# Kernel tuning notes

Measured on AMD Instinct MI355X. Metric: run time of the kernel, lower is better.

Reference implementation:

```python
import jax, jax.numpy as jnp
import numpy as np

# Module constants from CheckboxDetector.__init__ / _postprocess
N = 8192            # candidate detections
C = 2               # checkbox classes (checked / unchecked)
THR = 0.7           # confidence threshold (self.threshold)
IOU_THR = 0.5       # torchvision.ops.nms iou_threshold
INPUT_H, INPUT_W = 1280.0, 1280.0   # self.input_shape
IMG_H, IMG_W = 2480.0, 3508.0       # original image (A4 @ 300dpi)
SCALER = max(IMG_W / INPUT_W, IMG_H / INPUT_H)
EPS = 1e-9


def setup_inputs() -> dict:
    key = jax.random.key(0)
    k1, k2, k3 = jax.random.split(key, 3)
    cls_conf = jax.random.uniform(k1, (N, C), dtype=jnp.float32)
    # well-formed xyxy boxes inside the 1280x1280 canvas
    xy = jax.random.uniform(k2, (N, 2), dtype=jnp.float32, minval=0.0, maxval=1200.0)
    wh = jax.random.uniform(k3, (N, 2), dtype=jnp.float32, minval=8.0, maxval=80.0)
    bboxes = jnp.concatenate([xy, xy + wh], axis=1)  # [N,4]
    return {"cls_conf": cls_conf, "bboxes": bboxes}


def _pairwise_iou(boxes):
    # boxes: [N,4] xyxy -> iou: [N,N]
    x1, y1, x2, y2 = boxes[:, 0], boxes[:, 1], boxes[:, 2], boxes[:, 3]
    area = (x2 - x1) * (y2 - y1)
    iw = jnp.clip(jnp.minimum(x2[:, None], x2[None, :]) - jnp.maximum(x1[:, None], x1[None, :]), 0.0)
    ih = jnp.clip(jnp.minimum(y2[:, None], y2[None, :]) - jnp.maximum(y1[:, None], y1[None, :]), 0.0)
    inter = iw * ih
    return inter / (area[:, None] + area[None, :] - inter + EPS)


def reference(cls_conf, bboxes):
    # _threshold: keep rows with any class confidence > THR (mask instead of
    # dynamic filtering, for fixed shapes under jit)
    valid = jnp.any(cls_conf > THR, axis=1)            # [N]
    scores = jnp.max(cls_conf, axis=1)                 # cls_conf.max(1)
    masked_scores = jnp.where(valid, scores, -jnp.inf)

    # _nms: sort by score desc, greedy IoU suppression (torchvision semantics)
    order = jnp.argsort(-masked_scores)
    b = bboxes[order]          # [N,4]
    c = cls_conf[order]        # [N,C]
    v = valid[order]           # [N]

    iou = _pairwise_iou(b)     # [N,N]  (256 MB: memory-bound core)
    idx = jnp.arange(N)

    def body(i, keep):
        # box i (if still kept & valid) suppresses later boxes overlapping > IOU_THR
        sup = (iou[i] > IOU_THR) & (idx > i) & keep[i]
        return keep & ~sup

    keep = jax.lax.fori_loop(0, N, body, v)            # [N] bool

    # _postprocess tail: rescale boxes to original image size; suppressed
    # detections are zeroed (mask semantics in place of dynamic gather).
    kf = keep.astype(cls_conf.dtype)[:, None]
    boxes_out = b * SCALER * kf                        # [N,4]
    conf_out = c * kf                                  # [N,C]
    return jnp.concatenate([boxes_out, conf_out], axis=1)  # [N, 4+C]
```

## Files before the change

### kernel.cpp

```cpp
#include <hip/hip_runtime.h>
#include <math.h>

#define N_BOX 8192
#define NW 128
#define LCAP 24576
#define ECAP_MAX (1 << 21)
#define NCH 8
#define CH 1024
#define THR_C 0.7f
#define IOU_THR_C 0.5f
#define EPS_C 1e-9f

__device__ __constant__ float kScaler = (float)(3508.0 / 1280.0);

static __device__ __forceinline__ unsigned long long make_key(const float* conf, int i) {
    float c0 = conf[2 * i], c1 = conf[2 * i + 1];
    bool valid = (c0 > THR_C) || (c1 > THR_C);
    float ms = valid ? fmaxf(c0, c1) : -INFINITY;
    unsigned int u = __float_as_uint(ms);
    unsigned int m = (u & 0x80000000u) ? ~u : (u | 0x80000000u);
    unsigned int d = ~m;
    return ((unsigned long long)d << 32) | (unsigned int)i;
}

__global__ __launch_bounds__(256) void key_kernel(const float* __restrict__ conf,
                                                  unsigned long long* __restrict__ keys,
                                                  int* __restrict__ ecntE,
                                                  int* __restrict__ nvD) {
    int i = blockIdx.x * 256 + threadIdx.x;
    if (i == 0) { *ecntE = 0; *nvD = 0; }
    keys[i] = make_key(conf, i);
}

__global__ __launch_bounds__(256) void rank_kernel(const unsigned long long* __restrict__ keys,
                                                   int* __restrict__ partial) {
    int i = blockIdx.x * 256 + threadIdx.x;
    unsigned long long ki = keys[i];
    const ulonglong4* kp = (const ulonglong4*)(keys + blockIdx.y * CH);
    int c0 = 0, c1 = 0, c2 = 0, c3 = 0;
#pragma unroll 4
    for (int l = 0; l < CH / 4; ++l) {
        ulonglong4 kq = kp[l];
        c0 += (kq.x < ki) ? 1 : 0;
        c1 += (kq.y < ki) ? 1 : 0;
        c2 += (kq.z < ki) ? 1 : 0;
        c3 += (kq.w < ki) ? 1 : 0;
    }
    partial[blockIdx.y * N_BOX + i] = (c0 + c1) + (c2 + c3);
}

__global__ __launch_bounds__(256) void scatter_kernel(const float* __restrict__ conf,
                                                      const float* __restrict__ bboxes,
                                                      const int* __restrict__ partial,
                                                      float4* __restrict__ sb,
                                                      unsigned int* __restrict__ order,
                                                      int* __restrict__ nvD) {
    int i = blockIdx.x * 256 + threadIdx.x;
    int r = 0;
#pragma unroll
    for (int c = 0; c < NCH; ++c) r += partial[c * N_BOX + i];
    float c0 = conf[2 * i], c1 = conf[2 * i + 1];
    bool valid = (c0 > THR_C) || (c1 > THR_C);
    if (valid) {
        sb[r] = ((const float4*)bboxes)[i];
        order[r] = (unsigned int)i;
    }
    unsigned long long vb = __ballot(valid);
    if ((threadIdx.x & 63) == 0) atomicAdd(nvD, __popcll(vb));
}

__global__ void pair_kernel(const float4* __restrict__ sb,
                            const int* __restrict__ nvD,
                            unsigned int* __restrict__ edges,
                            int* __restrict__ ecntE,
                            int ecap) {
    int w = blockIdx.y;
    int jbase = w << 6;
    int ibase = blockIdx.x * 256;
    int nv = *nvD;
    if (ibase >= nv || jbase >= nv || jbase + 63 <= ibase) return;
    __shared__ float4 cb[64];
    __shared__ float carea[64];
    if (threadIdx.x < 64) {
        float4 c = sb[jbase + threadIdx.x];
        cb[threadIdx.x] = c;
        carea[threadIdx.x] = (c.z - c.x) * (c.w - c.y);
    }
    __syncthreads();
    int i = ibase + threadIdx.x;
    unsigned long long bits = 0ull;
    if (i < nv && jbase + 63 > i) {
        float4 r = sb[i];
        float ra = (r.z - r.x) * (r.w - r.y);
#pragma unroll 8
        for (int b = 0; b < 64; ++b) {
            float4 c = cb[b];
            float iw = fminf(r.z, c.z) - fmaxf(r.x, c.x);
            float ih = fminf(r.w, c.w) - fmaxf(r.y, c.y);
            iw = fmaxf(iw, 0.0f);
            ih = fmaxf(ih, 0.0f);
            float inter = iw * ih;
            float iou = inter / (ra + carea[b] - inter + EPS_C);
            if ((iou > IOU_THR_C) && ((jbase + b) > i)) bits |= (1ull << b);
        }
    }
    unsigned long long tmask = (jbase + 64 <= nv) ? ~0ull
                               : ((1ull << (nv - jbase)) - 1ull);
    unsigned long long ebits = bits & tmask;
    int lane = threadIdx.x & 63;
    int ec = __popcll(ebits);
    int pre = ec;
#pragma unroll
    for (int d = 1; d < 64; d <<= 1) {
        int vv = __shfl_up(pre, d, 64);
        if (lane >= d) pre += vv;
    }
    int tot = __shfl(pre, 63, 64);
    if (tot > 0) {
        int base = 0;
        if (lane == 63) base = atomicAdd(ecntE, tot);
        base = __shfl(base, 63, 64);
        int idx = base + pre - ec;
        unsigned long long tb = ebits;
        while (tb) {
            int b = __builtin_ctzll(tb); tb &= tb - 1;
            if (idx < ecap) edges[idx] = ((unsigned int)i << 13) | (unsigned int)(jbase + b);
            ++idx;
        }
    }
}

__global__ __launch_bounds__(512) void scan_kernel(const unsigned int* __restrict__ edges,
                                                   const int* __restrict__ ecntE,
                                                   const int* __restrict__ nvD,
                                                   const float4* __restrict__ sb,
                                                   unsigned long long* __restrict__ keepK,
                                                   int ecap) {
    __shared__ unsigned int eL[LCAP];
    __shared__ unsigned long long kL[NW], tL[NW], vL[NW];
    __shared__ int chg[3];
    int t = threadIdx.x;
    int cnt = *ecntE;
    int nv = *nvD;
    if (t < NW) {
        int lo = t << 6;
        unsigned long long v;
        if (nv >= lo + 64)      v = ~0ull;
        else if (nv <= lo)      v = 0ull;
        else                    v = (1ull << (nv - lo)) - 1ull;
        vL[t] = v; kL[t] = v;
    }
    if (t == 0) { chg[0] = 0; chg[1] = 0; chg[2] = 0; }
    if (cnt <= ecap) {
        int lim = cnt < LCAP ? cnt : LCAP;
        for (int e = t; e < lim; e += 512) eL[e] = edges[e];
    }
    __syncthreads();
    if (cnt <= ecap) {
        for (int it = 0; it < N_BOX; ++it) {
            if (t < NW) tL[t] = 0ull;
            __syncthreads();
            for (int e = t; e < cnt; e += 512) {
                unsigned int ed = (e < LCAP) ? eL[e] : edges[e];
                int src = (int)(ed >> 13);
                if ((kL[src >> 6] >> (src & 63)) & 1ull) {
                    int tg = (int)(ed & 8191u);
                    atomicOr(&tL[tg >> 6], 1ull << (tg & 63));
                }
            }
            __syncthreads();
            if (t < NW) {
                unsigned long long nk = vL[t] & ~tL[t];
                if (nk != kL[t]) chg[it % 3] = 1;
                kL[t] = nk;
            }
            if (t == 0) chg[(it + 2) % 3] = 0;
            __syncthreads();
            if (chg[it % 3] == 0) break;
        }
    } else {
        if (t < NW) tL[t] = 0ull;
        __syncthreads();
        if (t < 64) {
            int lane = t;
            for (int i = 0; i < nv - 1; ++i) {
                bool rem = (tL[i >> 6] >> (i & 63)) & 1ull;
                if (!rem) {
                    float4 r = sb[i];
                    float ra = (r.z - r.x) * (r.w - r.y);
                    for (int j = i + 1 + lane; j < nv; j += 64) {
                        float4 c = sb[j];
                        float ca = (c.z - c.x) * (c.w - c.y);
                        float iw = fminf(r.z, c.z) - fmaxf(r.x, c.x);
                        float ih = fminf(r.w, c.w) - fmaxf(r.y, c.y);
                        iw = fmaxf(iw, 0.0f);
                        ih = fmaxf(ih, 0.0f);
                        float inter = iw * ih;
                        float iou = inter / (ra + ca - inter + EPS_C);
                        if (iou > IOU_THR_C) atomicOr(&tL[j >> 6], 1ull << (j & 63));
                    }
                }
            }
        }
        __syncthreads();
        if (t < NW) kL[t] = vL[t] & ~tL[t];
    }
    __syncthreads();
    if (t < NW) keepK[t] = kL[t];
}

__global__ void out_kernel(const float4* __restrict__ sb,
                           const unsigned long long* __restrict__ keepK,
                           const unsigned int* __restrict__ order,
                           const float* __restrict__ conf,
                           float* __restrict__ out) {
    int i = blockIdx.x * 256 + threadIdx.x;
    bool kept = (keepK[i >> 6] >> (i & 63)) & 1ull;
    if (kept) {
        float4 b = sb[i];
        unsigned int o = order[i];
        out[i * 6 + 0] = b.x * kScaler;
        out[i * 6 + 1] = b.y * kScaler;
        out[i * 6 + 2] = b.z * kScaler;
        out[i * 6 + 3] = b.w * kScaler;
        out[i * 6 + 4] = conf[2 * o];
        out[i * 6 + 5] = conf[2 * o + 1];
    } else {
        out[i * 6 + 0] = 0.0f;
        out[i * 6 + 1] = 0.0f;
        out[i * 6 + 2] = 0.0f;
        out[i * 6 + 3] = 0.0f;
        out[i * 6 + 4] = 0.0f;
        out[i * 6 + 5] = 0.0f;
    }
}

extern "C" void kernel_launch(void* const* d_in, const int* in_sizes, int n_in,
                              void* d_out, int out_size, void* d_ws, size_t ws_size,
                              hipStream_t stream) {
    const float* cls_conf = (const float*)d_in[0];
    const float* bboxes   = (const float*)d_in[1];
    float* out = (float*)d_out;

    char* ws = (char*)d_ws;
    unsigned long long* keys    = (unsigned long long*)(ws + 0);
    int*                partial = (int*)(ws + 65536);
    float4*             sb      = (float4*)(ws + 327680);
    unsigned int*       order   = (unsigned int*)(ws + 458752);
    int*                ecntE   = (int*)(ws + 491520);
    int*                nvD     = (int*)(ws + 491524);
    unsigned long long* keepK   = (unsigned long long*)(ws + 492032);
    const size_t EDGE_OFF = 493568;
    unsigned int*       edges   = (unsigned int*)(ws + EDGE_OFF);
    size_t avail = (ws_size > EDGE_OFF + 16) ? (ws_size - EDGE_OFF) / 4 : 0;
    int ecap = (int)(avail > (size_t)ECAP_MAX ? (size_t)ECAP_MAX : avail);

    key_kernel<<<N_BOX / 256, 256, 0, stream>>>(cls_conf, keys, ecntE, nvD);
    rank_kernel<<<dim3(N_BOX / 256, NCH), 256, 0, stream>>>(keys, partial);
    scatter_kernel<<<N_BOX / 256, 256, 0, stream>>>(cls_conf, bboxes, partial, sb, order, nvD);
    pair_kernel<<<dim3(32, 128), 256, 0, stream>>>(sb, nvD, edges, ecntE, ecap);
    scan_kernel<<<1, 512, 0, stream>>>(edges, ecntE, nvD, sb, keepK, ecap);
    out_kernel<<<N_BOX / 256, 256, 0, stream>>>(sb, keepK, order, cls_conf, out);
}
```

Baseline: 116.8 us.

## Fuse six NMS kernels into one cooperative kernel with grid syncs

Replaces the six-kernel launch chain (key, rank, scatter, pair, scan, out) with a single cooperative kernel of 128 blocks × 512 threads that separates the stages with grid.sync(). The aim is to remove per-launch overhead and inter-kernel gaps in a pipeline made of many tiny stages. In exchange, each stage now runs on fewer threads with a different work split (the pair stage uses 128 blocks instead of 4096), and grid-wide barriers cost something. If the cooperative launch fails, the code falls back to the original six launches.

```diff
diff --git a/kernel.cpp b/kernel.cpp
--- a/kernel.cpp
+++ b/kernel.cpp
@@ -1,10 +1,15 @@
 #include <hip/hip_runtime.h>
+#include <hip/hip_cooperative_groups.h>
 #include <math.h>
+
+namespace cg = cooperative_groups;
 
 #define N_BOX 8192
 #define NW 128
 #define LCAP 24576
 #define ECAP_MAX (1 << 21)
+#define NBLK 128
+#define NTHR 512
 #define NCH 8
 #define CH 1024
 #define THR_C 0.7f
@@ -21,6 +26,224 @@
     unsigned int m = (u & 0x80000000u) ? ~u : (u | 0x80000000u);
     unsigned int d = ~m;
     return ((unsigned long long)d << 32) | (unsigned int)i;
+}
+
+__global__ __launch_bounds__(NTHR, 1) void fused_kernel(
+    const float* __restrict__ conf,
+    const float* __restrict__ bboxes,
+    float* __restrict__ out,
+    unsigned long long* __restrict__ keys,
+    int* __restrict__ partial,
+    float4* __restrict__ sb,
+    unsigned int* __restrict__ order,
+    unsigned int* __restrict__ edges,
+    int* __restrict__ ecntE,
+    int* __restrict__ nvD,
+    unsigned long long* __restrict__ keepK,
+    int ecap)
+{
+    cg::grid_group grid = cg::this_grid();
+
+    __shared__ unsigned int eL[LCAP];
+    __shared__ unsigned long long kL[NW], tL[NW], vL[NW];
+    __shared__ int chg[3];
+    __shared__ float4 cb[64];
+    __shared__ float carea[64];
+
+    const int t = threadIdx.x;
+    const int b = blockIdx.x;
+    const int tid = b * NTHR + t;
+
+    if (tid < N_BOX) keys[tid] = make_key(conf, tid);
+    if (tid == 0) { *ecntE = 0; *nvD = 0; }
+    grid.sync();
+
+    {
+        const int by = b & (NCH - 1);
+        const int bx = b >> 3;
+        const int i = bx * NTHR + t;
+        const unsigned long long ki = keys[i];
+        const ulonglong4* kp = (const ulonglong4*)(keys + by * CH);
+        int c0 = 0, c1 = 0, c2 = 0, c3 = 0;
+#pragma unroll 4
+        for (int l = 0; l < CH / 4; ++l) {
+            ulonglong4 kq = kp[l];
+            c0 += (kq.x < ki) ? 1 : 0;
+            c1 += (kq.y < ki) ? 1 : 0;
+            c2 += (kq.z < ki) ? 1 : 0;
+            c3 += (kq.w < ki) ? 1 : 0;
+        }
+        partial[by * N_BOX + i] = (c0 + c1) + (c2 + c3);
+    }
+    grid.sync();
+
+    if (tid < N_BOX) {
+        int r = 0;
+#pragma unroll
+        for (int c = 0; c < NCH; ++c) r += partial[c * N_BOX + tid];
+        float c0 = conf[2 * tid], c1 = conf[2 * tid + 1];
+        bool valid = (c0 > THR_C) || (c1 > THR_C);
+        if (valid) {
+            sb[r] = ((const float4*)bboxes)[tid];
+            order[r] = (unsigned int)tid;
+        }
+        unsigned long long vb = __ballot(valid);
+        if ((t & 63) == 0) atomicAdd(nvD, __popcll(vb));
+    }
+    grid.sync();
+
+    const int nv = *nvD;
+
+    {
+        const int jbase = b << 6;
+        if (jbase < nv) {
+            if (t < 64) {
+                float4 c = sb[jbase + t];
+                cb[t] = c;
+                carea[t] = (c.z - c.x) * (c.w - c.y);
+            }
+            __syncthreads();
+            for (int ib = 0; ib < 16; ++ib) {
+                int ibase = ib << 9;
+                if (ibase >= nv) break;
+                if (jbase + 63 <= ibase) continue;
+                int i = ibase + t;
+                unsigned long long bits = 0ull;
+                if (i < nv && jbase + 63 > i) {
+                    float4 r = sb[i];
+                    float ra = (r.z - r.x) * (r.w - r.y);
+#pragma unroll 8
+                    for (int bb = 0; bb < 64; ++bb) {
+                        float4 c = cb[bb];
+                        float iw = fminf(r.z, c.z) - fmaxf(r.x, c.x);
+                        float ih = fminf(r.w, c.w) - fmaxf(r.y, c.y);
+                        iw = fmaxf(iw, 0.0f);
+                        ih = fmaxf(ih, 0.0f);
+                        float inter = iw * ih;
+                        float iou = inter / (ra + carea[bb] - inter + EPS_C);
+                        if ((iou > IOU_THR_C) && ((jbase + bb) > i)) bits |= (1ull << bb);
+                    }
+                }
+                unsigned long long tmask = (jbase + 64 <= nv) ? ~0ull
+                                           : ((1ull << (nv - jbase)) - 1ull);
+                unsigned long long ebits = bits & tmask;
+                int lane = t & 63;
+                int ec = __popcll(ebits);
+                int pre = ec;
+#pragma unroll
+                for (int d = 1; d < 64; d <<= 1) {
+                    int vv = __shfl_up(pre, d, 64);
+                    if (lane >= d) pre += vv;
+                }
+                int tot = __shfl(pre, 63, 64);
+                if (tot > 0) {
+                    int base = 0;
+                    if (lane == 63) base = atomicAdd(ecntE, tot);
+                    base = __shfl(base, 63, 64);
+                    int idx = base + pre - ec;
+                    unsigned long long tb = ebits;
+                    while (tb) {
+                        int bb = __builtin_ctzll(tb); tb &= tb - 1;
+                        if (idx < ecap)
+                            edges[idx] = ((unsigned int)i << 13) | (unsigned int)(jbase + bb);
+                        ++idx;
+                    }
+                }
+            }
+        }
+    }
+    grid.sync();
+
+    if (b == 0) {
+        const int cnt = *ecntE;
+        if (t < NW) {
+            int lo = t << 6;
+            unsigned long long v;
+            if (nv >= lo + 64)      v = ~0ull;
+            else if (nv <= lo)      v = 0ull;
+            else                    v = (1ull << (nv - lo)) - 1ull;
+            vL[t] = v; kL[t] = v;
+        }
+        if (t == 0) { chg[0] = 0; chg[1] = 0; chg[2] = 0; }
+        if (cnt <= ecap) {
+            int lim = cnt < LCAP ? cnt : LCAP;
+            for (int e = t; e < lim; e += NTHR) eL[e] = edges[e];
+        }
+        __syncthreads();
+        if (cnt <= ecap) {
+            for (int it = 0; it < N_BOX; ++it) {
+                if (t < NW) tL[t] = 0ull;
+                __syncthreads();
+                for (int e = t; e < cnt; e += NTHR) {
+                    unsigned int ed = (e < LCAP) ? eL[e] : edges[e];
+                    int src = (int)(ed >> 13);
+                    if ((kL[src >> 6] >> (src & 63)) & 1ull) {
+                        int tg = (int)(ed & 8191u);
+                        atomicOr(&tL[tg >> 6], 1ull << (tg & 63));
+                    }
+                }
+                __syncthreads();
+                if (t < NW) {
+                    unsigned long long nk = vL[t] & ~tL[t];
+                    if (nk != kL[t]) chg[it % 3] = 1;
+                    kL[t] = nk;
+                }
+                if (t == 0) chg[(it + 2) % 3] = 0;
+                __syncthreads();
+                if (chg[it % 3] == 0) break;
+            }
+        } else {
+            if (t < NW) tL[t] = 0ull;
+            __syncthreads();
+            if (t < 64) {
+                int lane = t;
+                for (int i = 0; i < nv - 1; ++i) {
+                    bool rem = (tL[i >> 6] >> (i & 63)) & 1ull;
+                    if (!rem) {
+                        float4 r = sb[i];
+                        float ra = (r.z - r.x) * (r.w - r.y);
+                        for (int j = i + 1 + lane; j < nv; j += 64) {
+                            float4 c = sb[j];
+                            float ca = (c.z - c.x) * (c.w - c.y);
+                            float iw = fminf(r.z, c.z) - fmaxf(r.x, c.x);
+                            float ih = fminf(r.w, c.w) - fmaxf(r.y, c.y);
+                            iw = fmaxf(iw, 0.0f);
+                            ih = fmaxf(ih, 0.0f);
+                            float inter = iw * ih;
+                            float iou = inter / (ra + ca - inter + EPS_C);
+                            if (iou > IOU_THR_C) atomicOr(&tL[j >> 6], 1ull << (j & 63));
+                        }
+                    }
+                }
+            }
+            __syncthreads();
+            if (t < NW) kL[t] = vL[t] & ~tL[t];
+        }
+        __syncthreads();
+        if (t < NW) keepK[t] = kL[t];
+    }
+    grid.sync();
+
+    if (tid < N_BOX) {
+        bool kept = (keepK[tid >> 6] >> (tid & 63)) & 1ull;
+        if (kept) {
+            float4 bx = sb[tid];
+            unsigned int o = order[tid];
+            out[tid * 6 + 0] = bx.x * kScaler;
+            out[tid * 6 + 1] = bx.y * kScaler;
+            out[tid * 6 + 2] = bx.z * kScaler;
+            out[tid * 6 + 3] = bx.w * kScaler;
+            out[tid * 6 + 4] = conf[2 * o];
+            out[tid * 6 + 5] = conf[2 * o + 1];
+        } else {
+            out[tid * 6 + 0] = 0.0f;
+            out[tid * 6 + 1] = 0.0f;
+            out[tid * 6 + 2] = 0.0f;
+            out[tid * 6 + 3] = 0.0f;
+            out[tid * 6 + 4] = 0.0f;
+            out[tid * 6 + 5] = 0.0f;
+        }
+    }
 }
 
 __global__ __launch_bounds__(256) void key_kernel(const float* __restrict__ conf,
@@ -255,10 +478,19 @@
     size_t avail = (ws_size > EDGE_OFF + 16) ? (ws_size - EDGE_OFF) / 4 : 0;
     int ecap = (int)(avail > (size_t)ECAP_MAX ? (size_t)ECAP_MAX : avail);
 
-    key_kernel<<<N_BOX / 256, 256, 0, stream>>>(cls_conf, keys, ecntE, nvD);
-    rank_kernel<<<dim3(N_BOX / 256, NCH), 256, 0, stream>>>(keys, partial);
-    scatter_kernel<<<N_BOX / 256, 256, 0, stream>>>(cls_conf, bboxes, partial, sb, order, nvD);
-    pair_kernel<<<dim3(32, 128), 256, 0, stream>>>(sb, nvD, edges, ecntE, ecap);
-    scan_kernel<<<1, 512, 0, stream>>>(edges, ecntE, nvD, sb, keepK, ecap);
-    out_kernel<<<N_BOX / 256, 256, 0, stream>>>(sb, keepK, order, cls_conf, out);
-}
+    void* args[] = { (void*)&cls_conf, (void*)&bboxes, (void*)&out,
+                     (void*)&keys, (void*)&partial, (void*)&sb, (void*)&order,
+                     (void*)&edges, (void*)&ecntE, (void*)&nvD, (void*)&keepK,
+                     (void*)&ecap };
+    hipError_t err = hipLaunchCooperativeKernel((const void*)fused_kernel,
+                                                dim3(NBLK), dim3(NTHR),
+                                                args, 0, stream);
+    if (err != hipSuccess) {
+        key_kernel<<<N_BOX / 256, 256, 0, stream>>>(cls_conf, keys, ecntE, nvD);
+        rank_kernel<<<dim3(N_BOX / 256, NCH), 256, 0, stream>>>(keys, partial);
+        scatter_kernel<<<N_BOX / 256, 256, 0, stream>>>(cls_conf, bboxes, partial, sb, order, nvD);
+        pair_kernel<<<dim3(32, 128), 256, 0, stream>>>(sb, nvD, edges, ecntE, ecap);
+        scan_kernel<<<1, 512, 0, stream>>>(edges, ecntE, nvD, sb, keepK, ecap);
+        out_kernel<<<N_BOX / 256, 256, 0, stream>>>(sb, keepK, order, cls_conf, out);
+    }
+}
```

New measurement: 225.8 us. +93.3%, slower.

## Fuse NMS pipeline into two kernels with sort-free pair detection in original index space

Applied to the files above, without the earlier changes.

Replaces the six-kernel pipeline (key, rank, scatter, pair, scan, output) with two launches. Stage A runs pairwise IoU in original index order alongside the rank counting, orienting each edge by key comparison so the boxes do not need to be sorted first. Edges go into fixed per-wave slots instead of a global atomic counter. Stage B compacts the slots with a prefix sum, runs the iterative suppression and writes the output scattered by rank. This cuts launch and serialization overhead, but falls back to a slow serial path if any wave slot overflows or the edge count exceeds the shared-memory capacity.

```diff
diff --git a/kernel.cpp b/kernel.cpp
--- a/kernel.cpp
+++ b/kernel.cpp
@@ -3,18 +3,23 @@
 
 #define N_BOX 8192
 #define NW 128
+#define NTHR 512
 #define LCAP 24576
-#define ECAP_MAX (1 << 21)
+#define NPB 512
+#define ISPL 4
+#define NRB 128
+#define WPB 8
+#define NWAVE (NPB * WPB)
+#define SLOT 64
+#define WSPT (NWAVE / NTHR)
 #define NCH 8
-#define CH 1024
 #define THR_C 0.7f
 #define IOU_THR_C 0.5f
 #define EPS_C 1e-9f
 
 __device__ __constant__ float kScaler = (float)(3508.0 / 1280.0);
 
-static __device__ __forceinline__ unsigned long long make_key(const float* conf, int i) {
-    float c0 = conf[2 * i], c1 = conf[2 * i + 1];
+static __device__ __forceinline__ unsigned long long key_from(float c0, float c1, int i) {
     bool valid = (c0 > THR_C) || (c1 > THR_C);
     float ms = valid ? fmaxf(c0, c1) : -INFINITY;
     unsigned int u = __float_as_uint(ms);
@@ -23,145 +28,177 @@
     return ((unsigned long long)d << 32) | (unsigned int)i;
 }
 
-__global__ __launch_bounds__(256) void key_kernel(const float* __restrict__ conf,
-                                                  unsigned long long* __restrict__ keys,
-                                                  int* __restrict__ ecntE,
-                                                  int* __restrict__ nvD) {
-    int i = blockIdx.x * 256 + threadIdx.x;
-    if (i == 0) { *ecntE = 0; *nvD = 0; }
-    keys[i] = make_key(conf, i);
-}
-
-__global__ __launch_bounds__(256) void rank_kernel(const unsigned long long* __restrict__ keys,
-                                                   int* __restrict__ partial) {
-    int i = blockIdx.x * 256 + threadIdx.x;
-    unsigned long long ki = keys[i];
-    const ulonglong4* kp = (const ulonglong4*)(keys + blockIdx.y * CH);
-    int c0 = 0, c1 = 0, c2 = 0, c3 = 0;
+__global__ __launch_bounds__(NTHR) void stageA(const float* __restrict__ conf,
+                                               const float* __restrict__ bboxes,
+                                               int* __restrict__ partial,
+                                               unsigned int* __restrict__ wcnt,
+                                               unsigned int* __restrict__ wslot) {
+    int b = blockIdx.x;
+    int t = threadIdx.x;
+    if (b < NPB) {
+        __shared__ float4 cb[64];
+        __shared__ float carea[64];
+        __shared__ unsigned long long cbk[64];
+        __shared__ unsigned long long jvS;
+        int w = b >> 2;
+        int h = b & 3;
+        if (t < 64) {
+            int j = (w << 6) + t;
+            float4 c = ((const float4*)bboxes)[j];
+            cb[t] = c;
+            carea[t] = (c.z - c.x) * (c.w - c.y);
+            float c0 = conf[2 * j], c1 = conf[2 * j + 1];
+            cbk[t] = key_from(c0, c1, j);
+            unsigned long long bv = __ballot((c0 > THR_C) || (c1 > THR_C));
+            if (t == 0) jvS = bv;
+        }
+        __syncthreads();
+        unsigned long long jv = jvS;
+        int waveid = b * WPB + (t >> 6);
+        int lane = t & 63;
+        int wc = 0;
+        int jmax = (w << 6) + 63;
+        int ntiles = (jmax + NTHR) / NTHR;
+        for (int tt = h; tt < ntiles; tt += ISPL) {
+            int i = tt * NTHR + t;
+            unsigned long long bits = 0ull;
+            unsigned long long ki = 0ull;
+            int rel = i - (w << 6);
+            unsigned long long jm = jv;
+            if (rel >= 63) jm = 0ull;
+            else if (rel >= 0) jm &= ~((2ull << rel) - 1ull);
+            if (jm) {
+                float c0 = conf[2 * i], c1 = conf[2 * i + 1];
+                bool iv = (c0 > THR_C) || (c1 > THR_C);
+                if (iv) {
+                    ki = key_from(c0, c1, i);
+                    float4 r = ((const float4*)bboxes)[i];
+                    float ra = (r.z - r.x) * (r.w - r.y);
+#pragma unroll 8
+                    for (int bb = 0; bb < 64; ++bb) {
+                        float4 c = cb[bb];
+                        float iw = fminf(r.z, c.z) - fmaxf(r.x, c.x);
+                        float ih = fminf(r.w, c.w) - fmaxf(r.y, c.y);
+                        iw = fmaxf(iw, 0.0f);
+                        ih = fmaxf(ih, 0.0f);
+                        float inter = iw * ih;
+                        float iou = inter / (ra + carea[bb] - inter + EPS_C);
+                        if (iou > IOU_THR_C) bits |= (1ull << bb);
+                    }
+                    bits &= jm;
+                }
+            }
+            int ec = __popcll(bits);
+            int pre = ec;
+#pragma unroll
+            for (int d = 1; d < 64; d <<= 1) {
+                int vv = __shfl_up(pre, d, 64);
+                if (lane >= d) pre += vv;
+            }
+            int tot = __shfl(pre, 63, 64);
+            if (tot > 0) {
+                int idx = wc + pre - ec;
+                unsigned long long tb = bits;
+                while (tb) {
+                    int bb = __builtin_ctzll(tb); tb &= tb - 1;
+                    if (idx < SLOT) {
+                        int j = (w << 6) + bb;
+                        unsigned int e = (ki < cbk[bb])
+                                         ? (((unsigned int)i << 13) | (unsigned int)j)
+                                         : (((unsigned int)j << 13) | (unsigned int)i);
+                        wslot[(size_t)waveid * SLOT + idx] = e;
+                    }
+                    ++idx;
+                }
+                wc += tot;
+            }
+        }
+        if (lane == 0) wcnt[waveid] = (unsigned int)wc;
+    } else {
+        __shared__ unsigned long long ck[1024];
+        int rb = b - NPB;
+        int ech = rb >> 3;
+        int cch = rb & 7;
+        for (int l = t; l < 1024; l += NTHR) {
+            int j = (cch << 10) + l;
+            ck[l] = key_from(conf[2 * j], conf[2 * j + 1], j);
+        }
+        __syncthreads();
+        int i = (ech << 9) + t;
+        unsigned long long ki = key_from(conf[2 * i], conf[2 * i + 1], i);
+        const ulonglong2* ckp = (const ulonglong2*)ck;
+        int a0 = 0, a1 = 0, a2 = 0, a3 = 0;
 #pragma unroll 4
-    for (int l = 0; l < CH / 4; ++l) {
-        ulonglong4 kq = kp[l];
-        c0 += (kq.x < ki) ? 1 : 0;
-        c1 += (kq.y < ki) ? 1 : 0;
-        c2 += (kq.z < ki) ? 1 : 0;
-        c3 += (kq.w < ki) ? 1 : 0;
-    }
-    partial[blockIdx.y * N_BOX + i] = (c0 + c1) + (c2 + c3);
-}
-
-__global__ __launch_bounds__(256) void scatter_kernel(const float* __restrict__ conf,
-                                                      const float* __restrict__ bboxes,
-                                                      const int* __restrict__ partial,
-                                                      float4* __restrict__ sb,
-                                                      unsigned int* __restrict__ order,
-                                                      int* __restrict__ nvD) {
-    int i = blockIdx.x * 256 + threadIdx.x;
-    int r = 0;
-#pragma unroll
-    for (int c = 0; c < NCH; ++c) r += partial[c * N_BOX + i];
-    float c0 = conf[2 * i], c1 = conf[2 * i + 1];
-    bool valid = (c0 > THR_C) || (c1 > THR_C);
-    if (valid) {
-        sb[r] = ((const float4*)bboxes)[i];
-        order[r] = (unsigned int)i;
-    }
-    unsigned long long vb = __ballot(valid);
-    if ((threadIdx.x & 63) == 0) atomicAdd(nvD, __popcll(vb));
-}
-
-__global__ void pair_kernel(const float4* __restrict__ sb,
-                            const int* __restrict__ nvD,
-                            unsigned int* __restrict__ edges,
-                            int* __restrict__ ecntE,
-                            int ecap) {
-    int w = blockIdx.y;
-    int jbase = w << 6;
-    int ibase = blockIdx.x * 256;
-    int nv = *nvD;
-    if (ibase >= nv || jbase >= nv || jbase + 63 <= ibase) return;
-    __shared__ float4 cb[64];
-    __shared__ float carea[64];
-    if (threadIdx.x < 64) {
-        float4 c = sb[jbase + threadIdx.x];
-        cb[threadIdx.x] = c;
-        carea[threadIdx.x] = (c.z - c.x) * (c.w - c.y);
-    }
-    __syncthreads();
-    int i = ibase + threadIdx.x;
-    unsigned long long bits = 0ull;
-    if (i < nv && jbase + 63 > i) {
-        float4 r = sb[i];
-        float ra = (r.z - r.x) * (r.w - r.y);
-#pragma unroll 8
-        for (int b = 0; b < 64; ++b) {
-            float4 c = cb[b];
-            float iw = fminf(r.z, c.z) - fmaxf(r.x, c.x);
-            float ih = fminf(r.w, c.w) - fmaxf(r.y, c.y);
-            iw = fmaxf(iw, 0.0f);
-            ih = fmaxf(ih, 0.0f);
-            float inter = iw * ih;
-            float iou = inter / (ra + carea[b] - inter + EPS_C);
-            if ((iou > IOU_THR_C) && ((jbase + b) > i)) bits |= (1ull << b);
-        }
-    }
-    unsigned long long tmask = (jbase + 64 <= nv) ? ~0ull
-                               : ((1ull << (nv - jbase)) - 1ull);
-    unsigned long long ebits = bits & tmask;
-    int lane = threadIdx.x & 63;
-    int ec = __popcll(ebits);
-    int pre = ec;
-#pragma unroll
-    for (int d = 1; d < 64; d <<= 1) {
-        int vv = __shfl_up(pre, d, 64);
-        if (lane >= d) pre += vv;
-    }
-    int tot = __shfl(pre, 63, 64);
-    if (tot > 0) {
-        int base = 0;
-        if (lane == 63) base = atomicAdd(ecntE, tot);
-        base = __shfl(base, 63, 64);
-        int idx = base + pre - ec;
-        unsigned long long tb = ebits;
-        while (tb) {
-            int b = __builtin_ctzll(tb); tb &= tb - 1;
-            if (idx < ecap) edges[idx] = ((unsigned int)i << 13) | (unsigned int)(jbase + b);
-            ++idx;
-        }
-    }
-}
-
-__global__ __launch_bounds__(512) void scan_kernel(const unsigned int* __restrict__ edges,
-                                                   const int* __restrict__ ecntE,
-                                                   const int* __restrict__ nvD,
-                                                   const float4* __restrict__ sb,
-                                                   unsigned long long* __restrict__ keepK,
-                                                   int ecap) {
+        for (int l = 0; l < 512; l += 2) {
+            ulonglong2 u = ckp[l];
+            ulonglong2 v = ckp[l + 1];
+            a0 += (u.x < ki) ? 1 : 0;
+            a1 += (u.y < ki) ? 1 : 0;
+            a2 += (v.x < ki) ? 1 : 0;
+            a3 += (v.y < ki) ? 1 : 0;
+        }
+        partial[cch * N_BOX + i] = (a0 + a1) + (a2 + a3);
+    }
+}
+
+__global__ __launch_bounds__(NTHR) void stageB(const float* __restrict__ conf,
+                                               const float* __restrict__ bboxes,
+                                               const int* __restrict__ partial,
+                                               const unsigned int* __restrict__ wcnt,
+                                               const unsigned int* __restrict__ wslot,
+                                               float* __restrict__ out) {
     __shared__ unsigned int eL[LCAP];
     __shared__ unsigned long long kL[NW], tL[NW], vL[NW];
+    __shared__ int wsum[NTHR];
     __shared__ int chg[3];
+    __shared__ int fbF, nvF;
     int t = threadIdx.x;
-    int cnt = *ecntE;
-    int nv = *nvD;
-    if (t < NW) {
-        int lo = t << 6;
-        unsigned long long v;
-        if (nv >= lo + 64)      v = ~0ull;
-        else if (nv <= lo)      v = 0ull;
-        else                    v = (1ull << (nv - lo)) - 1ull;
-        vL[t] = v; kL[t] = v;
-    }
-    if (t == 0) { chg[0] = 0; chg[1] = 0; chg[2] = 0; }
-    if (cnt <= ecap) {
-        int lim = cnt < LCAP ? cnt : LCAP;
-        for (int e = t; e < lim; e += 512) eL[e] = edges[e];
-    }
-    __syncthreads();
-    if (cnt <= ecap) {
+    if (t == 0) { fbF = 0; nvF = 0; chg[0] = 0; chg[1] = 0; chg[2] = 0; }
+    for (int base = 0; base < N_BOX; base += NTHR) {
+        int i = base + t;
+        float c0 = conf[2 * i], c1 = conf[2 * i + 1];
+        unsigned long long bv = __ballot((c0 > THR_C) || (c1 > THR_C));
+        if ((t & 63) == 0) vL[i >> 6] = bv;
+    }
+    int nq[WSPT], myo[WSPT];
+    int s = 0;
+    bool ov = false;
+#pragma unroll
+    for (int q = 0; q < WSPT; ++q) {
+        int v = (int)wcnt[t * WSPT + q];
+        nq[q] = v; myo[q] = s; s += v;
+        if (v > SLOT) ov = true;
+    }
+    wsum[t] = s;
+    __syncthreads();
+    if (t < NW) kL[t] = vL[t];
+    for (int off = 1; off < NTHR; off <<= 1) {
+        int v = (t >= off) ? wsum[t - off] : 0;
+        __syncthreads();
+        wsum[t] += v;
+        __syncthreads();
+    }
+    int ebase = wsum[t] - s;
+    int totE = wsum[NTHR - 1];
+    if (ov || totE > LCAP) fbF = 1;
+    __syncthreads();
+    int fb = fbF;
+    if (!fb) {
+#pragma unroll
+        for (int q = 0; q < WSPT; ++q) {
+            int w2 = t * WSPT + q;
+            int off = ebase + myo[q];
+            for (int k = 0; k < nq[q]; ++k)
+                eL[off + k] = wslot[(size_t)w2 * SLOT + k];
+        }
+    }
+    __syncthreads();
+    if (!fb) {
         for (int it = 0; it < N_BOX; ++it) {
             if (t < NW) tL[t] = 0ull;
             __syncthreads();
-            for (int e = t; e < cnt; e += 512) {
-                unsigned int ed = (e < LCAP) ? eL[e] : edges[e];
+            for (int e = t; e < totE; e += NTHR) {
+                unsigned int ed = eL[e];
                 int src = (int)(ed >> 13);
                 if ((kL[src >> 6] >> (src & 63)) & 1ull) {
                     int tg = (int)(ed & 8191u);
@@ -179,17 +216,25 @@
             if (chg[it % 3] == 0) break;
         }
     } else {
-        if (t < NW) tL[t] = 0ull;
-        __syncthreads();
+        unsigned int* sinv = eL;
+        for (int base = 0; base < N_BOX; base += NTHR) {
+            int i = base + t;
+            int r = 0;
+#pragma unroll
+            for (int c = 0; c < NCH; ++c) r += partial[c * N_BOX + i];
+            sinv[r] = (unsigned int)i;
+        }
+        if (t < NW) { atomicAdd(&nvF, __popcll(vL[t])); tL[t] = 0ull; kL[t] = 0ull; }
+        __syncthreads();
+        int nv = nvF;
         if (t < 64) {
-            int lane = t;
-            for (int i = 0; i < nv - 1; ++i) {
-                bool rem = (tL[i >> 6] >> (i & 63)) & 1ull;
+            for (int a = 0; a < nv - 1; ++a) {
+                bool rem = (tL[a >> 6] >> (a & 63)) & 1ull;
                 if (!rem) {
-                    float4 r = sb[i];
+                    float4 r = ((const float4*)bboxes)[sinv[a]];
                     float ra = (r.z - r.x) * (r.w - r.y);
-                    for (int j = i + 1 + lane; j < nv; j += 64) {
-                        float4 c = sb[j];
+                    for (int b2 = a + 1 + t; b2 < nv; b2 += 64) {
+                        float4 c = ((const float4*)bboxes)[sinv[b2]];
                         float ca = (c.z - c.x) * (c.w - c.y);
                         float iw = fminf(r.z, c.z) - fmaxf(r.x, c.x);
                         float ih = fminf(r.w, c.w) - fmaxf(r.y, c.y);
@@ -197,41 +242,42 @@
                         ih = fmaxf(ih, 0.0f);
                         float inter = iw * ih;
                         float iou = inter / (ra + ca - inter + EPS_C);
-                        if (iou > IOU_THR_C) atomicOr(&tL[j >> 6], 1ull << (j & 63));
+                        if (iou > IOU_THR_C) atomicOr(&tL[b2 >> 6], 1ull << (b2 & 63));
                     }
                 }
             }
         }
         __syncthreads();
-        if (t < NW) kL[t] = vL[t] & ~tL[t];
-    }
-    __syncthreads();
-    if (t < NW) keepK[t] = kL[t];
-}
-
-__global__ void out_kernel(const float4* __restrict__ sb,
-                           const unsigned long long* __restrict__ keepK,
-                           const unsigned int* __restrict__ order,
-                           const float* __restrict__ conf,
-                           float* __restrict__ out) {
-    int i = blockIdx.x * 256 + threadIdx.x;
-    bool kept = (keepK[i >> 6] >> (i & 63)) & 1ull;
-    if (kept) {
-        float4 b = sb[i];
-        unsigned int o = order[i];
-        out[i * 6 + 0] = b.x * kScaler;
-        out[i * 6 + 1] = b.y * kScaler;
-        out[i * 6 + 2] = b.z * kScaler;
-        out[i * 6 + 3] = b.w * kScaler;
-        out[i * 6 + 4] = conf[2 * o];
-        out[i * 6 + 5] = conf[2 * o + 1];
-    } else {
-        out[i * 6 + 0] = 0.0f;
-        out[i * 6 + 1] = 0.0f;
-        out[i * 6 + 2] = 0.0f;
-        out[i * 6 + 3] = 0.0f;
-        out[i * 6 + 4] = 0.0f;
-        out[i * 6 + 5] = 0.0f;
+        for (int a = t; a < nv; a += NTHR) {
+            if (!((tL[a >> 6] >> (a & 63)) & 1ull)) {
+                int ia = (int)sinv[a];
+                atomicOr(&kL[ia >> 6], 1ull << (ia & 63));
+            }
+        }
+    }
+    __syncthreads();
+    for (int base = 0; base < N_BOX; base += NTHR) {
+        int i = base + t;
+        int r = 0;
+#pragma unroll
+        for (int c = 0; c < NCH; ++c) r += partial[c * N_BOX + i];
+        bool kept = (kL[i >> 6] >> (i & 63)) & 1ull;
+        if (kept) {
+            float4 bx = ((const float4*)bboxes)[i];
+            out[r * 6 + 0] = bx.x * kScaler;
+            out[r * 6 + 1] = bx.y * kScaler;
+            out[r * 6 + 2] = bx.z * kScaler;
+            out[r * 6 + 3] = bx.w * kScaler;
+            out[r * 6 + 4] = conf[2 * i];
+            out[r * 6 + 5] = conf[2 * i + 1];
+        } else {
+            out[r * 6 + 0] = 0.0f;
+            out[r * 6 + 1] = 0.0f;
+            out[r * 6 + 2] = 0.0f;
+            out[r * 6 + 3] = 0.0f;
+            out[r * 6 + 4] = 0.0f;
+            out[r * 6 + 5] = 0.0f;
+        }
     }
 }
 
@@ -243,22 +289,11 @@
     float* out = (float*)d_out;
 
     char* ws = (char*)d_ws;
-    unsigned long long* keys    = (unsigned long long*)(ws + 0);
-    int*                partial = (int*)(ws + 65536);
-    float4*             sb      = (float4*)(ws + 327680);
-    unsigned int*       order   = (unsigned int*)(ws + 458752);
-    int*                ecntE   = (int*)(ws + 491520);
-    int*                nvD     = (int*)(ws + 491524);
-    unsigned long long* keepK   = (unsigned long long*)(ws + 492032);
-    const size_t EDGE_OFF = 493568;
-    unsigned int*       edges   = (unsigned int*)(ws + EDGE_OFF);
-    size_t avail = (ws_size > EDGE_OFF + 16) ? (ws_size - EDGE_OFF) / 4 : 0;
-    int ecap = (int)(avail > (size_t)ECAP_MAX ? (size_t)ECAP_MAX : avail);
-
-    key_kernel<<<N_BOX / 256, 256, 0, stream>>>(cls_conf, keys, ecntE, nvD);
-    rank_kernel<<<dim3(N_BOX / 256, NCH), 256, 0, stream>>>(keys, partial);
-    scatter_kernel<<<N_BOX / 256, 256, 0, stream>>>(cls_conf, bboxes, partial, sb, order, nvD);
-    pair_kernel<<<dim3(32, 128), 256, 0, stream>>>(sb, nvD, edges, ecntE, ecap);
-    scan_kernel<<<1, 512, 0, stream>>>(edges, ecntE, nvD, sb, keepK, ecap);
-    out_kernel<<<N_BOX / 256, 256, 0, stream>>>(sb, keepK, order, cls_conf, out);
-}
+    int*          partial = (int*)(ws + 0);
+    unsigned int* wcnt    = (unsigned int*)(ws + 262144);
+    unsigned int* wslot   = (unsigned int*)(ws + 278528);
+    (void)ws_size; (void)in_sizes; (void)n_in; (void)out_size;
+
+    stageA<<<NPB + NRB, NTHR, 0, stream>>>(cls_conf, bboxes, partial, wcnt, wslot);
+    stageB<<<1, NTHR, 0, stream>>>(cls_conf, bboxes, partial, wcnt, wslot, out);
+}
```

New measurement: 129.8 us. 1.11x slower.
